# Optimization experiments

Hardware: AMD Instinct MI355X
Metric: run time of the kernel (lower is better)

## Reference

```python
import jax, jax.numpy as jnp
import numpy as np

R = 7          # region_size
BW = 2.5       # KDE bandwidth
EPS = 1e-8

def _blur5x5(x):
    # AvgPool2d(kernel=5, stride=1, padding=2, count_include_pad=True)
    s = jax.lax.reduce_window(x, 0.0, jax.lax.add, (1, 1, 5, 5), (1, 1, 1, 1),
                              [(0, 0), (0, 0), (2, 2), (2, 2)])
    return s / 25.0

def setup_inputs() -> dict:
    key = jax.random.key(0)
    x = jax.random.uniform(key, (2, 2, 1, 80, 80), dtype=jnp.float32) * 255.0
    return {"x": x}

def reference(x):
    N, SF, C, H, W = x.shape
    B = N * SF
    xi = x.reshape(B, C, H, W)

    # unsharp-mask style preprocessing (round/clamp as in torch)
    smooth = jnp.round(_blur5x5(xi))
    sharp = jnp.round(jnp.clip(2.5 * xi - 1.25 * smooth, 0.0, 255.0))
    division = jnp.round(jnp.clip(sharp * 255.0 / (smooth + EPS), 0.0, 255.0))

    Hp, Wp = H - R + 1, W - R + 1
    L = R * R
    # overlapping RxR patches: (B, C*R*R, Hp, Wp), features ordered (C, R, R)
    patches = jax.lax.conv_general_dilated_patches(division, (R, R), (1, 1), 'VALID')
    patches = patches.reshape(B, C, L, Hp * Wp).transpose(0, 3, 2, 1)  # (B, P, L, C)

    # KDE-based local entropy: p_i = mean_j N(x_i - x_j; 0, BW^2 I_C)
    d2 = jnp.sum((patches[:, :, :, None, :] - patches[:, :, None, :, :]) ** 2, axis=-1)  # (B,P,L,L)
    inv2b2 = 1.0 / (2.0 * BW * BW)
    norm = (2.0 * np.pi * BW * BW) ** (C / 2.0)
    p = jnp.exp(-d2 * inv2b2).mean(axis=-1) / norm          # (B, P, L)
    ent = -jnp.mean(jnp.log(p + EPS), axis=-1)              # (B, P)

    ent = ent.reshape(B, Hp, Wp)
    pad = R // 2
    ent = jnp.pad(ent, ((0, 0), (pad, pad), (pad, pad)))    # back to (B, H, W)
    return ent.reshape(N, SF, H, W)
```

## Files before the change

kernel.cpp:

```cpp
#include <hip/hip_runtime.h>
#include <math.h>

#define BATCH 4
#define H 80
#define W 80
#define R 7
#define L 49
#define PAD 3
#define TILES_X 40
#define TILES 1600

__device__ __forceinline__ float clamp255(float v) {
    return fminf(fmaxf(v, 0.0f), 255.0f);
}

__global__ void preprocess_kernel(const float* __restrict__ x, float* __restrict__ divimg) {
    int idx = blockIdx.x * blockDim.x + threadIdx.x;
    if (idx >= BATCH * H * W) return;
    int b  = idx / (H * W);
    int r  = idx % (H * W);
    int y  = r / W;
    int xc = r % W;
    const float* img = x + b * H * W;

    double s = 0.0;
    #pragma unroll
    for (int dy = -2; dy <= 2; ++dy) {
        int yy = y + dy;
        if (yy < 0 || yy >= H) continue;
        #pragma unroll
        for (int dx = -2; dx <= 2; ++dx) {
            int xx = xc + dx;
            if (xx < 0 || xx >= W) continue;
            s += (double)img[yy * W + xx];
        }
    }
    float smooth = rintf((float)(s / 25.0));
    float xv = img[y * W + xc];
    float sharp = rintf(clamp255(__fsub_rn(__fmul_rn(2.5f, xv), __fmul_rn(1.25f, smooth))));
    float dv = rintf(clamp255(__fdiv_rn(__fmul_rn(sharp, 255.0f), __fadd_rn(smooth, 1e-8f))));
    divimg[idx] = dv;
}

__global__ void entropy_kernel(const float* __restrict__ divimg, float* __restrict__ out) {
    const float KSCALE = 0.33972871239731236f;
    const float PSCALE = 1.0f / (49.0f * 6.266570686577501f);
    const float EPS    = 1e-8f;
    const float LN2_49 = 0.6931471805599453f / 49.0f;

    int gtid = blockIdx.x * blockDim.x + threadIdx.x;
    int wave = gtid >> 6;
    int lane = threadIdx.x & 63;
    if (wave >= BATCH * TILES) return;

    int b   = wave / TILES;
    int rem = wave % TILES;
    int ty  = rem / TILES_X;
    int tx  = rem % TILES_X;
    int oy0 = 2 * ty;
    int ox0 = 2 * tx;

    int lr = lane >> 3;
    int lc = lane & 7;
    int iy = oy0 - PAD + lr;  iy = iy < 0 ? 0 : (iy > H - 1 ? H - 1 : iy);
    int ix = ox0 - PAD + lc;  ix = ix < 0 ? 0 : (ix > W - 1 ? W - 1 : ix);
    float u = divimg[b * H * W + iy * W + ix] * KSCALE;

    float a00 = 0.0f, a01 = 0.0f, a10 = 0.0f, a11 = 0.0f;
    #pragma unroll
    for (int j = 0; j < 64; ++j) {
        float uj = __uint_as_float(__builtin_amdgcn_readlane(__float_as_uint(u), j));
        float s  = u - uj;
        float e  = __builtin_amdgcn_exp2f(-(s * s));
        int rj = j >> 3, cj = j & 7;
        if (rj < 7 && cj < 7) a00 += e;
        if (rj < 7 && cj >= 1) a01 += e;
        if (rj >= 1 && cj < 7) a10 += e;
        if (rj >= 1 && cj >= 1) a11 += e;
    }

    float t00 = (lr < 7 && lc < 7) ? __builtin_amdgcn_logf(fmaf(a00, PSCALE, EPS)) : 0.0f;
    float t01 = (lr < 7 && lc >= 1) ? __builtin_amdgcn_logf(fmaf(a01, PSCALE, EPS)) : 0.0f;
    float t10 = (lr >= 1 && lc < 7) ? __builtin_amdgcn_logf(fmaf(a10, PSCALE, EPS)) : 0.0f;
    float t11 = (lr >= 1 && lc >= 1) ? __builtin_amdgcn_logf(fmaf(a11, PSCALE, EPS)) : 0.0f;
    #pragma unroll
    for (int off = 32; off; off >>= 1) {
        t00 += __shfl_xor(t00, off, 64);
        t01 += __shfl_xor(t01, off, 64);
        t10 += __shfl_xor(t10, off, 64);
        t11 += __shfl_xor(t11, off, 64);
    }

    if (lane == 0) {
        float* outb = out + b * H * W;
        int oy1 = oy0 + 1, ox1 = ox0 + 1;
        bool iy0ok = (oy0 >= PAD) && (oy0 < H - PAD);
        bool iy1ok = (oy1 >= PAD) && (oy1 < H - PAD);
        bool ix0ok = (ox0 >= PAD) && (ox0 < W - PAD);
        bool ix1ok = (ox1 >= PAD) && (ox1 < W - PAD);
        float2 row0, row1;
        row0.x = (iy0ok && ix0ok) ? -t00 * LN2_49 : 0.0f;
        row0.y = (iy0ok && ix1ok) ? -t01 * LN2_49 : 0.0f;
        row1.x = (iy1ok && ix0ok) ? -t10 * LN2_49 : 0.0f;
        row1.y = (iy1ok && ix1ok) ? -t11 * LN2_49 : 0.0f;
        *(float2*)(outb + oy0 * W + ox0) = row0;
        *(float2*)(outb + oy1 * W + ox0) = row1;
    }
}

extern "C" void kernel_launch(void* const* d_in, const int* in_sizes, int n_in,
                              void* d_out, int out_size, void* d_ws, size_t ws_size,
                              hipStream_t stream) {
    const float* x = (const float*)d_in[0];
    float* out = (float*)d_out;
    float* divimg = (float*)d_ws;

    preprocess_kernel<<<(BATCH * H * W + 255) / 256, 256, 0, stream>>>(x, divimg);

    entropy_kernel<<<(BATCH * TILES * 64 + 255) / 256, 256, 0, stream>>>(divimg, out);
}
```

Before: 66.92 us.

## Fuse preprocessing into entropy kernel and pack accumulators into packed float2 adds

Drops the separate preprocessing kernel: each lane now computes the blurred, sharpened, divided pixel value it needs directly from the input, removing one launch and the intermediate workspace round trip. The price is redundant recomputation, since each pixel is recomputed by many overlapping tiles, each doing a 25-tap double-precision sum. The four per-lane KDE accumulators are also packed into two float2 vectors so paired masks can use packed adds.

```diff
diff --git a/kernel.cpp b/kernel.cpp
--- a/kernel.cpp
+++ b/kernel.cpp
@@ -10,39 +10,13 @@
 #define TILES_X 40
 #define TILES 1600
 
+typedef float v2f __attribute__((ext_vector_type(2)));
+
 __device__ __forceinline__ float clamp255(float v) {
     return fminf(fmaxf(v, 0.0f), 255.0f);
 }
 
-__global__ void preprocess_kernel(const float* __restrict__ x, float* __restrict__ divimg) {
-    int idx = blockIdx.x * blockDim.x + threadIdx.x;
-    if (idx >= BATCH * H * W) return;
-    int b  = idx / (H * W);
-    int r  = idx % (H * W);
-    int y  = r / W;
-    int xc = r % W;
-    const float* img = x + b * H * W;
-
-    double s = 0.0;
-    #pragma unroll
-    for (int dy = -2; dy <= 2; ++dy) {
-        int yy = y + dy;
-        if (yy < 0 || yy >= H) continue;
-        #pragma unroll
-        for (int dx = -2; dx <= 2; ++dx) {
-            int xx = xc + dx;
-            if (xx < 0 || xx >= W) continue;
-            s += (double)img[yy * W + xx];
-        }
-    }
-    float smooth = rintf((float)(s / 25.0));
-    float xv = img[y * W + xc];
-    float sharp = rintf(clamp255(__fsub_rn(__fmul_rn(2.5f, xv), __fmul_rn(1.25f, smooth))));
-    float dv = rintf(clamp255(__fdiv_rn(__fmul_rn(sharp, 255.0f), __fadd_rn(smooth, 1e-8f))));
-    divimg[idx] = dv;
-}
-
-__global__ void entropy_kernel(const float* __restrict__ divimg, float* __restrict__ out) {
+__global__ void entropy_fused_kernel(const float* __restrict__ x, float* __restrict__ out) {
     const float KSCALE = 0.33972871239731236f;
     const float PSCALE = 1.0f / (49.0f * 6.266570686577501f);
     const float EPS    = 1e-8f;
@@ -64,25 +38,54 @@
     int lc = lane & 7;
     int iy = oy0 - PAD + lr;  iy = iy < 0 ? 0 : (iy > H - 1 ? H - 1 : iy);
     int ix = ox0 - PAD + lc;  ix = ix < 0 ? 0 : (ix > W - 1 ? W - 1 : ix);
-    float u = divimg[b * H * W + iy * W + ix] * KSCALE;
 
-    float a00 = 0.0f, a01 = 0.0f, a10 = 0.0f, a11 = 0.0f;
+    const float* img = x + b * H * W;
+
+    double s = 0.0;
+    float xv = 0.0f;
+    #pragma unroll
+    for (int dy = -2; dy <= 2; ++dy) {
+        int yy = iy + dy;
+        bool yok = (yy >= 0) & (yy < H);
+        #pragma unroll
+        for (int dx = -2; dx <= 2; ++dx) {
+            int xx = ix + dx;
+            if (yok && xx >= 0 && xx < W) {
+                float v = img[yy * W + xx];
+                if (dy == 0 && dx == 0) xv = v;
+                s += (double)v;
+            }
+        }
+    }
+    float smooth = rintf((float)(s / 25.0));
+    float sharp  = rintf(clamp255(__fsub_rn(__fmul_rn(2.5f, xv), __fmul_rn(1.25f, smooth))));
+    float dv     = rintf(clamp255(__fdiv_rn(__fmul_rn(sharp, 255.0f), __fadd_rn(smooth, 1e-8f))));
+    float u      = dv * KSCALE;
+
+    v2f aA = {0.0f, 0.0f};
+    v2f aB = {0.0f, 0.0f};
     #pragma unroll
     for (int j = 0; j < 64; ++j) {
         float uj = __uint_as_float(__builtin_amdgcn_readlane(__float_as_uint(u), j));
-        float s  = u - uj;
-        float e  = __builtin_amdgcn_exp2f(-(s * s));
-        int rj = j >> 3, cj = j & 7;
-        if (rj < 7 && cj < 7) a00 += e;
-        if (rj < 7 && cj >= 1) a01 += e;
-        if (rj >= 1 && cj < 7) a10 += e;
-        if (rj >= 1 && cj >= 1) a11 += e;
+        float d  = u - uj;
+        float e  = __builtin_amdgcn_exp2f(-(d * d));
+        const int rj = j >> 3, cj = j & 7;
+        const bool m00 = (rj < 7) && (cj < 7);
+        const bool m01 = (rj < 7) && (cj >= 1);
+        const bool m10 = (rj >= 1) && (cj < 7);
+        const bool m11 = (rj >= 1) && (cj >= 1);
+        if (m00 && m01)      { v2f ee = {e, e}; aA += ee; }
+        else if (m00)        aA.x += e;
+        else if (m01)        aA.y += e;
+        if (m10 && m11)      { v2f ee = {e, e}; aB += ee; }
+        else if (m10)        aB.x += e;
+        else if (m11)        aB.y += e;
     }
 
-    float t00 = (lr < 7 && lc < 7) ? __builtin_amdgcn_logf(fmaf(a00, PSCALE, EPS)) : 0.0f;
-    float t01 = (lr < 7 && lc >= 1) ? __builtin_amdgcn_logf(fmaf(a01, PSCALE, EPS)) : 0.0f;
-    float t10 = (lr >= 1 && lc < 7) ? __builtin_amdgcn_logf(fmaf(a10, PSCALE, EPS)) : 0.0f;
-    float t11 = (lr >= 1 && lc >= 1) ? __builtin_amdgcn_logf(fmaf(a11, PSCALE, EPS)) : 0.0f;
+    float t00 = (lr < 7 && lc < 7)  ? __builtin_amdgcn_logf(fmaf(aA.x, PSCALE, EPS)) : 0.0f;
+    float t01 = (lr < 7 && lc >= 1) ? __builtin_amdgcn_logf(fmaf(aA.y, PSCALE, EPS)) : 0.0f;
+    float t10 = (lr >= 1 && lc < 7) ? __builtin_amdgcn_logf(fmaf(aB.x, PSCALE, EPS)) : 0.0f;
+    float t11 = (lr >= 1 && lc >= 1)? __builtin_amdgcn_logf(fmaf(aB.y, PSCALE, EPS)) : 0.0f;
     #pragma unroll
     for (int off = 32; off; off >>= 1) {
         t00 += __shfl_xor(t00, off, 64);
@@ -113,9 +116,7 @@
                               hipStream_t stream) {
     const float* x = (const float*)d_in[0];
     float* out = (float*)d_out;
-    float* divimg = (float*)d_ws;
+    (void)d_ws; (void)ws_size;
 
-    preprocess_kernel<<<(BATCH * H * W + 255) / 256, 256, 0, stream>>>(x, divimg);
-
-    entropy_kernel<<<(BATCH * TILES * 64 + 255) / 256, 256, 0, stream>>>(divimg, out);
+    entropy_fused_kernel<<<(BATCH * TILES * 64 + 255) / 256, 256, 0, stream>>>(x, out);
 }
```

New measurement: 63.16 us. 5.6% less time.
